# Kernel optimization log

Measured on AMD Instinct MI355X. Metric: run time of the kernel, lower is better.

Reference implementation:

```python
import jax, jax.numpy as jnp
import numpy as np

NB, DM, DIN, DS, DTR, K = 4, 64, 128, 16, 4, 4
C, COUT, H, W, BATCH, NH = 256, 256, 32, 32, 4, 8


def layernorm(x, w, b, eps=1e-5):
    mu = x.mean(-1, keepdims=True)
    var = ((x - mu) ** 2).mean(-1, keepdims=True)
    return (x - mu) * jax.lax.rsqrt(var + eps) * w + b


def ln_hw(x, eps=1e-5):
    # F.layer_norm(x, [H, W]) -> normalize over last two dims, no affine
    mu = x.mean((-2, -1), keepdims=True)
    var = ((x - mu) ** 2).mean((-2, -1), keepdims=True)
    return (x - mu) * jax.lax.rsqrt(var + eps)


def conv1d(x, w, b, groups=1, pad=1):
    # x: (B, Cin, L), w: (Cout, Cin//groups, k)
    y = jax.lax.conv_general_dilated(x, w, (1,), [(pad, pad)],
                                     dimension_numbers=('NCH', 'OIH', 'NCH'),
                                     feature_group_count=groups)
    return y + b[None, :, None]


def selective_scan(u, dt, Bm, Cm, A, Dp):
    # u, dt: (B,L,din); Bm, Cm: (B,L,ds); A: (din,ds); Dp: (din,)
    dA = jnp.exp(dt[..., None] * A)                     # (B,L,din,ds)
    dBu = (dt * u)[..., None] * Bm[:, :, None, :]       # (B,L,din,ds)

    def step(h, inp):
        dA_t, dBu_t, C_t = inp
        h = dA_t * h + dBu_t
        return h, jnp.einsum('bds,bs->bd', h, C_t)

    h0 = jnp.zeros((u.shape[0], DIN, DS), u.dtype)
    _, ys = jax.lax.scan(step, h0, (dA.transpose(1, 0, 2, 3), dBu.transpose(1, 0, 2, 3), Cm.transpose(1, 0, 2)))
    return ys.transpose(1, 0, 2) + u * Dp


def mamba(xs, inw, convw, convb, xpw, dtw, dtb, alog, dp, outw):
    # xs: (B,L,DM) one branch of Mamba(d_model=DM, d_state=DS, d_conv=K, expand=2)
    xz = xs @ inw.T                                     # (B,L,2*DIN)
    u, z = jnp.split(xz, 2, axis=-1)
    # causal depthwise conv1d (torch pads K-1 and truncates to L == left pad K-1)
    uc = jax.lax.conv_general_dilated(u.transpose(0, 2, 1), convw[:, None, :], (1,), [(K - 1, 0)],
                                      dimension_numbers=('NCH', 'OIH', 'NCH'),
                                      feature_group_count=DIN) + convb[None, :, None]
    u = jax.nn.silu(uc.transpose(0, 2, 1))              # (B,L,DIN)
    xdbc = u @ xpw.T                                    # (B,L,DTR+2*DS)
    dt = jax.nn.softplus(xdbc[..., :DTR] @ dtw.T + dtb)
    Bm, Cm = xdbc[..., DTR:DTR + DS], xdbc[..., DTR + DS:]
    y = selective_scan(u, dt, Bm, Cm, -jnp.exp(alog), dp)
    return (y * jax.nn.silu(z)) @ outw.T


mamba_v = jax.vmap(mamba)  # over branch axis 0 of inputs and all params


def mha(x, inw, inb, outw, outb):
    B, N, Cc = x.shape
    hd = Cc // NH
    qkv = x @ inw.T + inb
    q, k, v = jnp.split(qkv, 3, axis=-1)
    q = q.reshape(B, N, NH, hd).transpose(0, 2, 1, 3)
    k = k.reshape(B, N, NH, hd).transpose(0, 2, 1, 3)
    v = v.reshape(B, N, NH, hd).transpose(0, 2, 1, 3)
    att = jax.nn.softmax((q @ k.transpose(0, 1, 3, 2)) * (1.0 / (hd ** 0.5)), axis=-1)
    o = (att @ v).transpose(0, 2, 1, 3).reshape(B, N, Cc)
    return o @ outw.T + outb


def reference(x, norm_w, norm_b, skip_scale, m_inw, m_convw, m_convb, m_xpw, m_dtw, m_dtb, m_alog, m_d, m_outw, qdw_w, qdw_b, qpw_w, qpw_b, rdw_w, rdw_b, rpw_w, rpw_b, fdw_w, fdw_b, fpw_w, fpw_b, lc_w, lc_b, attn_inw, attn_inb, attn_outw, attn_outb, lgn_w, lgn_b, fc_w, fc_b, dwc_w, dwc_b, proj_w, proj_b):
    B, Cc, Hh, Ww = x.shape
    N = Hh * Ww
    xs = x.reshape(B, Cc, N).transpose(0, 2, 1)         # (B,N,C)
    xn = layernorm(xs, norm_w, norm_b)
    # channel-chunk into NB branches: (NB,B,N,DM)
    xc = xn.reshape(B, N, NB, DM).transpose(2, 0, 1, 3)
    xm = mamba_v(xc, m_inw, m_convw, m_convb, m_xpw, m_dtw, m_dtb, m_alog, m_d, m_outw) + skip_scale * xc
    x_concat = xm.transpose(1, 2, 0, 3).reshape(B, N, Cc)
    # branch gating: depthwise grouped conv (C->NB) then pointwise (NB->NB)
    Q = conv1d(conv1d(x_concat.transpose(0, 2, 1), qdw_w, qdw_b, groups=NB, pad=1), qpw_w, qpw_b, groups=1, pad=0)
    g = jax.nn.sigmoid(Q)                               # (B,NB,N)
    xg = (g.transpose(1, 0, 2)[..., None] * xm).transpose(1, 2, 0, 3).reshape(B, N, Cc)
    xgt = xg.transpose(0, 2, 1)                          # (B,C,N)
    R = conv1d(conv1d(xgt, rdw_w, rdw_b, groups=Cc, pad=1), rpw_w, rpw_b, groups=1, pad=0) + xgt
    cat = jnp.concatenate([xs, R.transpose(0, 2, 1)], axis=-1).transpose(0, 2, 1)  # (B,2C,N)
    xm2 = conv1d(conv1d(cat, fdw_w, fdw_b, groups=2 * Cc, pad=1), fpw_w, fpw_b, groups=1, pad=0) + cat[:, :Cc, :]
    xm2 = xm2.transpose(0, 2, 1)                         # (B,N,C)
    # local-global feature mixing
    x_local = conv1d(xm2.transpose(0, 2, 1), lc_w, lc_b, groups=Cc, pad=1).transpose(0, 2, 1)
    x_global = mha(xm2, attn_inw, attn_inb, attn_outw, attn_outb)
    x_out = jnp.concatenate([x_local, x_global], axis=-1) @ fc_w.T + fc_b
    x_out = jax.nn.gelu(layernorm(x_out, lgn_w, lgn_b), approximate=False)
    # DepthwiseConvolution: layer_norm over [H,W] (no affine) then depthwise conv2d
    xi = x_out.transpose(0, 2, 1).reshape(B, Cc, Hh, Ww)
    xi = ln_hw(xi)
    xi = jax.lax.conv_general_dilated(xi, dwc_w, (1, 1), [(1, 1), (1, 1)],
                                      dimension_numbers=('NCHW', 'OIHW', 'NCHW'),
                                      feature_group_count=Cc) + dwc_b[None, :, None, None]
    x_mixed = xi.reshape(B, Cc, N).transpose(0, 2, 1)
    x_mixed = layernorm(x_mixed, norm_w, norm_b)        # self.norm reused
    x_mixed = x_mixed @ proj_w.T + proj_b
    return x_mixed.transpose(0, 2, 1).reshape(B, COUT, Hh, Ww)


def setup_inputs() -> dict:
    key = jax.random.key(0)
    ks = iter(jax.random.split(key, 64))

    def rn(shape, s=0.02):
        return jax.random.normal(next(ks), shape, jnp.float32) * s

    return dict(
        x=jax.random.normal(next(ks), (BATCH, C, H, W), jnp.float32),
        norm_w=jnp.ones((C,), jnp.float32), norm_b=jnp.zeros((C,), jnp.float32),
        skip_scale=jnp.ones((1,), jnp.float32),
        m_inw=rn((NB, 2 * DIN, DM)), m_convw=rn((NB, DIN, K), 0.2), m_convb=jnp.zeros((NB, DIN), jnp.float32),
        m_xpw=rn((NB, DTR + 2 * DS, DIN)), m_dtw=rn((NB, DIN, DTR), 0.2), m_dtb=rn((NB, DIN), 0.5),
        m_alog=jnp.tile(jnp.log(jnp.arange(1, DS + 1, dtype=jnp.float32)), (NB, DIN, 1)),
        m_d=jnp.ones((NB, DIN), jnp.float32), m_outw=rn((NB, DM, DIN)),
        qdw_w=rn((NB, C // NB, 3), 0.1), qdw_b=jnp.zeros((NB,), jnp.float32),
        qpw_w=rn((NB, NB, 1), 0.3), qpw_b=jnp.zeros((NB,), jnp.float32),
        rdw_w=rn((C, 1, 3), 0.2), rdw_b=jnp.zeros((C,), jnp.float32),
        rpw_w=rn((C, C, 1)), rpw_b=jnp.zeros((C,), jnp.float32),
        fdw_w=rn((2 * C, 1, 3), 0.2), fdw_b=jnp.zeros((2 * C,), jnp.float32),
        fpw_w=rn((C, 2 * C, 1)), fpw_b=jnp.zeros((C,), jnp.float32),
        lc_w=rn((C, 1, 3), 0.2), lc_b=jnp.zeros((C,), jnp.float32),
        attn_inw=rn((3 * C, C)), attn_inb=jnp.zeros((3 * C,), jnp.float32),
        attn_outw=rn((C, C)), attn_outb=jnp.zeros((C,), jnp.float32),
        lgn_w=jnp.ones((C,), jnp.float32), lgn_b=jnp.zeros((C,), jnp.float32),
        fc_w=rn((C, 2 * C)), fc_b=jnp.zeros((C,), jnp.float32),
        dwc_w=rn((C, 1, 3, 3), 0.2), dwc_b=jnp.zeros((C,), jnp.float32),
        proj_w=rn((COUT, C)), proj_b=jnp.zeros((COUT,), jnp.float32),
    )
```

## Files before the change

### kernel.cpp

```cpp
#include <hip/hip_runtime.h>
#include <math.h>


namespace {
constexpr int NB_ = 4, DM_ = 64, DIN_ = 128, DS_ = 16, DTR_ = 4;
constexpr int C_ = 256, N_ = 1024, B_ = 4, HD_ = 32;
constexpr int NCH = 16, LCH = 64;
constexpr int NSTATE = 16 * 128 * 16;
}

typedef __attribute__((ext_vector_type(8))) short bf16x8;
typedef __attribute__((ext_vector_type(4))) float f32x4;
typedef __attribute__((ext_vector_type(8))) unsigned short ushort8v;
typedef __attribute__((ext_vector_type(4))) unsigned short ushort4v;

__device__ __forceinline__ unsigned short f2b(float f) {
  unsigned int u = __float_as_uint(f);
  unsigned int r = u + 0x7FFFu + ((u >> 16) & 1u);
  return (unsigned short)(r >> 16);
}

__device__ __forceinline__ float siluf(float x) { return x / (1.f + expf(-x)); }
__device__ __forceinline__ float sigmf(float x) { return 1.f / (1.f + expf(-x)); }
__device__ __forceinline__ float softplusf(float x) {
  return fmaxf(x, 0.f) + log1pf(expf(-fabsf(x)));
}

__global__ __launch_bounds__(256) void k_ln_t2(const float* __restrict__ in,
                                               const float* __restrict__ w,
                                               const float* __restrict__ bias,
                                               float* __restrict__ out_ln,
                                               float* __restrict__ out_copy) {
  __shared__ float tile[256][17];
  __shared__ float redp[16][16][2];
  __shared__ float stats[16][2];
  int bx = blockIdx.x;
  int b = bx >> 6, n0 = (bx & 63) * 16;
  int c = threadIdx.x;
  {
    const float* p = in + ((long)(b * C_ + c)) * N_ + n0;
#pragma unroll
    for (int j = 0; j < 16; ++j) tile[c][j] = p[j];
  }
  __syncthreads();
  {
    int n = c & 15, g = c >> 4;
    float a = 0.f, q = 0.f;
#pragma unroll
    for (int i = 0; i < 16; ++i) {
      float v = tile[g * 16 + i][n];
      a += v; q += v * v;
    }
    redp[g][n][0] = a; redp[g][n][1] = q;
  }
  __syncthreads();
  if (c < 16) {
    float a = 0.f, q = 0.f;
#pragma unroll
    for (int g2 = 0; g2 < 16; ++g2) { a += redp[g2][c][0]; q += redp[g2][c][1]; }
    float mu = a * (1.f / C_);
    float rs = rsqrtf(q * (1.f / C_) - mu * mu + 1e-5f);
    stats[c][0] = mu; stats[c][1] = rs;
  }
  __syncthreads();
  float wv = w[c], bv = bias[c];
#pragma unroll
  for (int j = 0; j < 16; ++j) {
    float v = tile[c][j];
    long o = ((long)(b * N_ + n0 + j)) * C_ + c;
    if (out_copy) out_copy[o] = v;
    out_ln[o] = (v - stats[j][0]) * stats[j][1] * wv + bv;
  }
}

__global__ __launch_bounds__(256) void k_inproj_mfma(const float* __restrict__ xn,
                                                     const float* __restrict__ inw,
                                                     float* __restrict__ UPRE,
                                                     float* __restrict__ Z) {
  __shared__ unsigned short xa[64][72];
  __shared__ unsigned short wb[64][72];
  int r0 = blockIdx.x * 64;
  int nb = blockIdx.y >> 2, c0 = (blockIdx.y & 3) * 64;
  int t = threadIdx.x;
  int wv = t >> 6, lane = t & 63, g = lane >> 4, ql = lane & 15;
  const f32x4 zf = {0.f, 0.f, 0.f, 0.f};
  f32x4 acc[4] = {zf, zf, zf, zf};
  int rr = t >> 2, kq = (t & 3) * 16;
  {
    const float* xsrc = xn + (long)(r0 + rr) * C_ + nb * 64 + kq;
#pragma unroll
    for (int j = 0; j < 4; ++j) {
      float4 v = *(const float4*)(xsrc + 4 * j);
      ushort4v u = {f2b(v.x), f2b(v.y), f2b(v.z), f2b(v.w)};
      *(ushort4v*)&xa[rr][kq + 4 * j] = u;
    }
    const float* wsrc = inw + ((long)nb * 256 + c0 + rr) * 64 + kq;
#pragma unroll
    for (int j = 0; j < 4; ++j) {
      float4 v = *(const float4*)(wsrc + 4 * j);
      ushort4v u = {f2b(v.x), f2b(v.y), f2b(v.z), f2b(v.w)};
      *(ushort4v*)&wb[rr][kq + 4 * j] = u;
    }
// ... 23 lines not shown
__global__ __launch_bounds__(256) void k_causal(const float* __restrict__ Uin,
                                                float* __restrict__ Uout,
                                                const float* __restrict__ cw,
                                                const float* __restrict__ cb) {
  __shared__ float u_s[35][128];
  int bx = blockIdx.x;
  int nbb = bx >> 5, chk = bx & 31;
  int nb = nbb >> 2;
  int n0 = chk * 32;
  const float* ibase = Uin + (long)nbb * N_ * DIN_;
  float* obase = Uout + (long)nbb * N_ * DIN_;
  for (int i = threadIdx.x; i < 35 * 32; i += 256) {
    int row = i >> 5, q = i & 31;
    int n = n0 - 3 + row;
    float4 v = (n >= 0) ? *(const float4*)&ibase[(long)n * DIN_ + q * 4]
                        : make_float4(0.f, 0.f, 0.f, 0.f);
    *(float4*)&u_s[row][q * 4] = v;
  }
  __syncthreads();
  int d = threadIdx.x & 127, half = threadIdx.x >> 7;
  float w0 = cw[(nb * DIN_ + d) * 4 + 0], w1 = cw[(nb * DIN_ + d) * 4 + 1];
  float w2 = cw[(nb * DIN_ + d) * 4 + 2], w3 = cw[(nb * DIN_ + d) * 4 + 3];
  float bv = cb[nb * DIN_ + d];
#pragma unroll
  for (int j = 0; j < 16; ++j) {
    int nn = half * 16 + j;
    float acc = bv + w3 * u_s[nn + 3][d] + w2 * u_s[nn + 2][d] +
                w1 * u_s[nn + 1][d] + w0 * u_s[nn][d];
    obase[(long)(n0 + nn) * DIN_ + d] = siluf(acc);
  }
}

__global__ __launch_bounds__(256) void k_xdbc(const float* __restrict__ U,
                                              const float* __restrict__ xpw,
                                              const float* __restrict__ dtw,
                                              const float* __restrict__ dtb,
                                              float* __restrict__ DT,
                                              float* __restrict__ BMb, float* __restrict__ CMb) {
  __shared__ float wl[36][129];
  __shared__ float u16[16][129];
  __shared__ float xd_s[16][37];
  __shared__ float dtw_s[128][4];
  __shared__ float dtb_s[128];
  int t = threadIdx.x;
  long row0 = (long)blockIdx.x * 16;
  int nb = blockIdx.x >> 8;
  for (int i = t; i < 36 * 128; i += 256) wl[i >> 7][i & 127] = xpw[nb * 36 * 128 + i];
  for (int i = t; i < 16 * 128; i += 256) u16[i >> 7][i & 127] = U[(row0 + (i >> 7)) * DIN_ + (i & 127)];
  for (int i = t; i < 512; i += 256) dtw_s[i >> 2][i & 3] = dtw[nb * 512 + i];
  if (t < 128) dtb_s[t] = dtb[nb * DIN_ + t];
  __syncthreads();
  {
    int r = t >> 4, jl = t & 15;
    float a0 = 0.f, a1 = 0.f, a2 = 0.f;
    for (int k = 0; k < 128; ++k) {
      float uv = u16[r][k];
      a0 += uv * wl[jl][k];
      a1 += uv * wl[jl + 16][k];
      if (jl < 4) a2 += uv * wl[jl + 32][k];
    }
    xd_s[r][jl] = a0;
    xd_s[r][jl + 16] = a1;
    if (jl < 4) xd_s[r][jl + 32] = a2;
  }
  __syncthreads();
  {
    int r = t >> 4, s = t & 15;
    BMb[(row0 + r) * DS_ + s] = xd_s[r][4 + s];
    CMb[(row0 + r) * DS_ + s] = xd_s[r][20 + s];
  }
  {
    int r = t >> 4, dl = t & 15;
    float x0 = xd_s[r][0], x1 = xd_s[r][1], x2 = xd_s[r][2], x3 = xd_s[r][3];
#pragma unroll
    for (int dd = 0; dd < 8; ++dd) {
      int d = dl * 8 + dd;
      float a = dtb_s[d] + x0 * dtw_s[d][0] + x1 * dtw_s[d][1] +
                x2 * dtw_s[d][2] + x3 * dtw_s[d][3];
      DT[(row0 + r) * DIN_ + d] = softplusf(a);
    }
  }
}

__global__ __launch_bounds__(256) void k_scanA(const float* __restrict__ DT,
                                               const float* __restrict__ U,
                                               const float* __restrict__ BMb,
                                               const float* __restrict__ alog,
                                               float* __restrict__ Aprod,
                                               float* __restrict__ Hend) {
  __shared__ float dt_s[64][64];
  __shared__ float u_s[64][64];
  __shared__ float bm_s[64][16];
  int bx = blockIdx.x;
  int chunk = bx >> 5, rem = bx & 31, nbb = rem >> 1, dh = rem & 1;
  int nb = nbb >> 2;
  int t = threadIdx.x;
  int dl = t >> 2, sg = t & 3;
  int d = dh * 64 + dl;
  long base = (long)nbb * N_ + chunk * LCH;
#pragma unroll
  for (int j = 0; j < 4; ++j) {
    int f = t + 256 * j;
    int tt = f >> 4, dq = (f & 15) * 4;
    long src = (base + tt) * DIN_ + dh * 64 + dq;
    *(float4*)&dt_s[tt][dq] = *(const float4*)&DT[src];
    *(float4*)&u_s[tt][dq]  = *(const float4*)&U[src];
  }
  {
    int tt = t >> 2, sq = (t & 3) * 4;
    *(float4*)&bm_s[tt][sq] = *(const float4*)&BMb[(base + tt) * DS_ + sq];
  }
  float A[4];
#pragma unroll
  for (int i = 0; i < 4; ++i)
    A[i] = -expf(alog[(nb * DIN_ + d) * DS_ + sg * 4 + i]);
  __syncthreads();
  float h[4] = {0.f, 0.f, 0.f, 0.f};
  float ap[4] = {1.f, 1.f, 1.f, 1.f};
  for (int tt = 0; tt < LCH; ++tt) {
    float dtv = dt_s[tt][dl];
    float uv  = u_s[tt][dl];
    float cc = dtv * uv;
    float4 bm4 = *(const float4*)&bm_s[tt][sg * 4];
    float bmv[4] = {bm4.x, bm4.y, bm4.z, bm4.w};
#pragma unroll
    for (int i = 0; i < 4; ++i) {
      float dA = __expf(dtv * A[i]);
      h[i] = dA * h[i] + cc * bmv[i];
      ap[i] *= dA;
    }
  }
  long st = (long)chunk * NSTATE + ((nbb << 7) + d) * 16 + sg * 4;
  *(float4*)&Aprod[st] = make_float4(ap[0], ap[1], ap[2], ap[3]);
  *(float4*)&Hend[st]  = make_float4(h[0], h[1], h[2], h[3]);
}

__global__ __launch_bounds__(256) void k_scanB(float* __restrict__ Aprod,
                                               const float* __restrict__ Hend) {
  int state = blockIdx.x * 256 + threadIdx.x;
  float H = 0.f;
#pragma unroll
  for (int c = 0; c < NCH; ++c) {
    long idx = (long)c * NSTATE + state;
    float a = Aprod[idx];
    float e = Hend[idx];
    Aprod[idx] = H;
    H = e + a * H;
  }
}

__global__ __launch_bounds__(256) void k_scanC(float* __restrict__ DT,
                                               const float* __restrict__ U,
                                               const float* __restrict__ BMb,
                                               const float* __restrict__ CMb,
                                               const float* __restrict__ alog,
                                               const float* __restrict__ Dp,
                                               const float* __restrict__ Hin) {
  __shared__ float dt_s[64][64];
  __shared__ float u_s[64][64];
  __shared__ float bm_s[64][16];
  __shared__ float cm_s[64][16];
  int bx = blockIdx.x;
  int chunk = bx >> 5, rem = bx & 31, nbb = rem >> 1, dh = rem & 1;
  int nb = nbb >> 2;
  int t = threadIdx.x;
  int dl = t >> 2, sg = t & 3;
  int d = dh * 64 + dl;
  long base = (long)nbb * N_ + chunk * LCH;
#pragma unroll
  for (int j = 0; j < 4; ++j) {
    int f = t + 256 * j;
    int tt = f >> 4, dq = (f & 15) * 4;
    long src = (base + tt) * DIN_ + dh * 64 + dq;
    *(float4*)&dt_s[tt][dq] = *(const float4*)&DT[src];
    *(float4*)&u_s[tt][dq]  = *(const float4*)&U[src];
  }
  {
    int tt = t >> 2, sq = (t & 3) * 4;
    *(float4*)&bm_s[tt][sq] = *(const float4*)&BMb[(base + tt) * DS_ + sq];
    *(float4*)&cm_s[tt][sq] = *(const float4*)&CMb[(base + tt) * DS_ + sq];
  }
  float A[4];
#pragma unroll
  for (int i = 0; i < 4; ++i)
    A[i] = -expf(alog[(nb * DIN_ + d) * DS_ + sg * 4 + i]);
  float Dv = Dp[nb * DIN_ + d];
  float h[4];
  {
    long st = (long)chunk * NSTATE + ((nbb << 7) + d) * 16 + sg * 4;
    float4 h4 = *(const float4*)&Hin[st];
    h[0] = h4.x; h[1] = h4.y; h[2] = h4.z; h[3] = h4.w;
  }
  __syncthreads();
  for (int tt = 0; tt < LCH; ++tt) {
    float dtv = dt_s[tt][dl];
    float uv  = u_s[tt][dl];
    float cc = dtv * uv;
    float4 bm4 = *(const float4*)&bm_s[tt][sg * 4];
    float4 cm4 = *(const float4*)&cm_s[tt][sg * 4];
    float bmv[4] = {bm4.x, bm4.y, bm4.z, bm4.w};
    float cmv[4] = {cm4.x, cm4.y, cm4.z, cm4.w};
    float p = 0.f;
#pragma unroll
    for (int i = 0; i < 4; ++i) {
      float dA = __expf(dtv * A[i]);
      h[i] = dA * h[i] + cc * bmv[i];
      p += h[i] * cmv[i];
    }
    p += __shfl_xor(p, 1, 64);
    p += __shfl_xor(p, 2, 64);
    if (sg == 0) DT[(base + tt) * DIN_ + d] = p + Dv * uv;
  }
}

__global__ __launch_bounds__(256) void k_outproj_mfma(const float* __restrict__ Y,
                                                      const float* __restrict__ Zb,
                                                      const float* __restrict__ outw,
                                                      const float* __restrict__ xn,
                                                      const float* __restrict__ skip,
                                                      float* __restrict__ XMC) {
  __shared__ unsigned short xa[64][72];
  __shared__ unsigned short wb[64][72];
  int r0 = blockIdx.x * 64;
  int nb = blockIdx.y;
  int t = threadIdx.x;
  int wv = t >> 6, lane = t & 63, g = lane >> 4, ql = lane & 15;
  const f32x4 zf = {0.f, 0.f, 0.f, 0.f};
  f32x4 acc[4] = {zf, zf, zf, zf};
  int rr = t >> 2, kq = (t & 3) * 16;
  for (int k0 = 0; k0 < 128; k0 += 64) {
    __syncthreads();
    long row = (long)nb * 4096 + r0 + rr;
    const float* ysrc = Y + row * DIN_ + k0 + kq;
    const float* zsrc = Zb + row * DIN_ + k0 + kq;
#pragma unroll
    for (int j = 0; j < 4; ++j) {
      float4 yv = *(const float4*)(ysrc + 4 * j);
      float4 zv = *(const float4*)(zsrc + 4 * j);
      ushort4v u = {f2b(yv.x * siluf(zv.x)), f2b(yv.y * siluf(zv.y)),
                    f2b(yv.z * siluf(zv.z)), f2b(yv.w * siluf(zv.w))};
      *(ushort4v*)&xa[rr][kq + 4 * j] = u;
    }
    const float* wsrc = outw + ((long)nb * 64 + rr) * 128 + k0 + kq;
#pragma unroll
    for (int j = 0; j < 4; ++j) {
      float4 v = *(const float4*)(wsrc + 4 * j);
      ushort4v u = {f2b(v.x), f2b(v.y), f2b(v.z), f2b(v.w)};
      *(ushort4v*)&wb[rr][kq + 4 * j] = u;
    }
    __syncthreads();
#pragma unroll
    for (int ks = 0; ks < 2; ++ks) {
      bf16x8 a = *(const bf16x8*)&xa[wv * 16 + ql][ks * 32 + g * 8];
#pragma unroll
      for (int ct = 0; ct < 4; ++ct) {
        bf16x8 b = *(const bf16x8*)&wb[ct * 16 + ql][ks * 32 + g * 8];
        acc[ct] = __builtin_amdgcn_mfma_f32_16x16x32_bf16(a, b, acc[ct], 0, 0, 0);
      }
    }
  }
  float sk = skip[0];
#pragma unroll
  for (int ct = 0; ct < 4; ++ct) {
    int col = ct * 16 + ql;
#pragma unroll
    for (int reg = 0; reg < 4; ++reg) {
      int bn = r0 + wv * 16 + g * 4 + reg;
      long oc = (long)bn * C_ + nb * 64 + col;
      XMC[oc] = acc[ct][reg] + sk * xn[oc];
    }
  }
}

__global__ __launch_bounds__(256) void k_gate(const float* __restrict__ XMC,
                                              const float* __restrict__ qdw_w,
                                              const float* __restrict__ qdw_b,
                                              const float* __restrict__ qpw_w,
                                              const float* __restrict__ qpw_b,
                                              float* __restrict__ G) {
  int t = threadIdx.x;
  int gid = (blockIdx.x * 256 + t) >> 4;
  int cq = t & 3, p = (t >> 2) & 3;
  int b = gid >> 10, n = gid & 1023;
  float a = 0.f;
#pragma unroll
  for (int k = 0; k < 3; ++k) {
    int nn = n + k - 1;
    if (nn < 0 || nn >= N_) continue;
    const float* xr = XMC + ((long)b * N_ + nn) * C_ + p * 64 + cq * 16;
    const float* wr = qdw_w + (p * 64 + cq * 16) * 3 + k;
#pragma unroll
    for (int i = 0; i < 16; ++i) a += xr[i] * wr[i * 3];
  }
  a += __shfl_xor(a, 1, 64);
// ... 118 lines not shown
  }
}

template <int KD, bool TOUT>
__global__ __launch_bounds__(256) void k_gemm_rm(const float* __restrict__ inA,
                                                 const float* __restrict__ inB,
                                                 const float* __restrict__ w,
                                                 const float* __restrict__ bias,
                                                 float* __restrict__ out,
                                                 int Cout, int lda) {
  __shared__ unsigned short xa[64][72];
  __shared__ unsigned short wb[64][72];
  __shared__ float tt[TOUT ? 64 : 1][TOUT ? 68 : 1];
  int r0 = blockIdx.x * 64;
  int c0 = blockIdx.y * 64;
  int t = threadIdx.x;
  int wv = t >> 6, lane = t & 63, g = lane >> 4, ql = lane & 15;
  const f32x4 zf = {0.f, 0.f, 0.f, 0.f};
  f32x4 acc[4] = {zf, zf, zf, zf};
  int rr = t >> 2, kq = (t & 3) * 16;
  for (int k0 = 0; k0 < KD; k0 += 64) {
    __syncthreads();
    int kk = k0 + kq;
    const float* xsrc = (inB != nullptr && kk >= KD / 2)
                            ? inB + (long)(r0 + rr) * lda + (kk - KD / 2)
                            : inA + (long)(r0 + rr) * lda + kk;
#pragma unroll
    for (int j = 0; j < 4; ++j) {
      float4 v = *(const float4*)(xsrc + 4 * j);
      ushort4v u = {f2b(v.x), f2b(v.y), f2b(v.z), f2b(v.w)};
      *(ushort4v*)&xa[rr][kq + 4 * j] = u;
    }
    const float* wsrc = w + (long)(c0 + rr) * KD + kk;
#pragma unroll
    for (int j = 0; j < 4; ++j) {
      float4 v = *(const float4*)(wsrc + 4 * j);
      ushort4v u = {f2b(v.x), f2b(v.y), f2b(v.z), f2b(v.w)};
      *(ushort4v*)&wb[rr][kq + 4 * j] = u;
    }
    __syncthreads();
#pragma unroll
    for (int ks = 0; ks < 2; ++ks) {
      bf16x8 a = *(const bf16x8*)&xa[wv * 16 + ql][ks * 32 + g * 8];
#pragma unroll
      for (int ct = 0; ct < 4; ++ct) {
        bf16x8 b = *(const bf16x8*)&wb[ct * 16 + ql][ks * 32 + g * 8];
        acc[ct] = __builtin_amdgcn_mfma_f32_16x16x32_bf16(a, b, acc[ct], 0, 0, 0);
      }
    }
  }
  if constexpr (!TOUT) {
#pragma unroll
    for (int ct = 0; ct < 4; ++ct) {
      int col = c0 + ct * 16 + ql;
      float bv = bias[col];
#pragma unroll
      for (int reg = 0; reg < 4; ++reg) {
        long row = r0 + wv * 16 + g * 4 + reg;
        out[row * Cout + col] = acc[ct][reg] + bv;
      }
    }
  } else {
#pragma unroll
    for (int ct = 0; ct < 4; ++ct) {
      int col = ct * 16 + ql;
      float bv = bias[c0 + col];
#pragma unroll
      for (int reg = 0; reg < 4; ++reg)
        tt[col][wv * 16 + g * 4 + reg] = acc[ct][reg] + bv;
    }
    __syncthreads();
    int b = r0 >> 10, n0 = r0 & 1023;
    int col = t >> 2, nq = (t & 3) * 16;
    float* op = out + ((long)(b * 256 + c0 + col)) * 1024 + n0 + nq;
#pragma unroll
    for (int j = 0; j < 4; ++j) {
      float4 v = make_float4(tt[col][nq + 4 * j], tt[col][nq + 4 * j + 1],
                             tt[col][nq + 4 * j + 2], tt[col][nq + 4 * j + 3]);
      *(float4*)(op + 4 * j) = v;
    }
  }
}

__global__ __launch_bounds__(256) void k_gemm_fc(const float* __restrict__ XM2,
                                                 const float* __restrict__ XGL,
                                                 const float* __restrict__ lcw,
                                                 const float* __restrict__ lcb,
                                                 const float* __restrict__ w,
                                                 const float* __restrict__ bias,
                                                 float* __restrict__ out) {
  __shared__ unsigned short xa[64][72];
  __shared__ unsigned short wb[64][72];
  int r0 = blockIdx.x * 64;
  int c0 = blockIdx.y * 64;
  int t = threadIdx.x;
  int wv = t >> 6, lane = t & 63, g = lane >> 4, ql = lane & 15;
  const f32x4 zf = {0.f, 0.f, 0.f, 0.f};
  f32x4 acc[4] = {zf, zf, zf, zf};
  int rr = t >> 2, kq = (t & 3) * 16;
  for (int k0 = 0; k0 < 512; k0 += 64) {
    __syncthreads();
    int kk = k0 + kq;
    long row = r0 + rr;
    if (kk < 256) {
      int n = (int)(row & 1023);
      const float* pc = XM2 + row * 256 + kk;
      bool hm = n > 0, hp = n < 1023;
#pragma unroll
      for (int j = 0; j < 4; ++j) {
        float4 v = *(const float4*)(pc + 4 * j);
        float4 vm = hm ? *(const float4*)(pc - 256 + 4 * j) : make_float4(0.f, 0.f, 0.f, 0.f);
        float4 vp = hp ? *(const float4*)(pc + 256 + 4 * j) : make_float4(0.f, 0.f, 0.f, 0.f);
        int c = kk + 4 * j;
        xa[rr][kq + 4 * j + 0] = f2b(lcb[c + 0] + lcw[(c + 0) * 3] * vm.x + lcw[(c + 0) * 3 + 1] * v.x + lcw[(c + 0) * 3 + 2] * vp.x);
        xa[rr][kq + 4 * j + 1] = f2b(lcb[c + 1] + lcw[(c + 1) * 3] * vm.y + lcw[(c + 1) * 3 + 1] * v.y + lcw[(c + 1) * 3 + 2] * vp.y);
        xa[rr][kq + 4 * j + 2] = f2b(lcb[c + 2] + lcw[(c + 2) * 3] * vm.z + lcw[(c + 2) * 3 + 1] * v.z + lcw[(c + 2) * 3 + 2] * vp.z);
        xa[rr][kq + 4 * j + 3] = f2b(lcb[c + 3] + lcw[(c + 3) * 3] * vm.w + lcw[(c + 3) * 3 + 1] * v.w + lcw[(c + 3) * 3 + 2] * vp.w);
      }
    } else {
      const float* xsrc = XGL + row * 256 + (kk - 256);
#pragma unroll
      for (int j = 0; j < 4; ++j) {
        float4 v = *(const float4*)(xsrc + 4 * j);
        ushort4v u = {f2b(v.x), f2b(v.y), f2b(v.z), f2b(v.w)};
        *(ushort4v*)&xa[rr][kq + 4 * j] = u;
      }
    }
    const float* wsrc = w + (long)(c0 + rr) * 512 + kk;
#pragma unroll
    for (int j = 0; j < 4; ++j) {
      float4 v = *(const float4*)(wsrc + 4 * j);
      ushort4v u = {f2b(v.x), f2b(v.y), f2b(v.z), f2b(v.w)};
      *(ushort4v*)&wb[rr][kq + 4 * j] = u;
    }
    __syncthreads();
#pragma unroll
    for (int ks = 0; ks < 2; ++ks) {
      bf16x8 a = *(const bf16x8*)&xa[wv * 16 + ql][ks * 32 + g * 8];
#pragma unroll
      for (int ct = 0; ct < 4; ++ct) {
        bf16x8 b = *(const bf16x8*)&wb[ct * 16 + ql][ks * 32 + g * 8];
        acc[ct] = __builtin_amdgcn_mfma_f32_16x16x32_bf16(a, b, acc[ct], 0, 0, 0);
      }
    }
  }
#pragma unroll
  for (int ct = 0; ct < 4; ++ct) {
    int col = c0 + ct * 16 + ql;
    float bv = bias[col];
#pragma unroll
    for (int reg = 0; reg < 4; ++reg) {
      long row = r0 + wv * 16 + g * 4 + reg;
      out[row * 256 + col] = acc[ct][reg] + bv;
    }
  }
}

__global__ __launch_bounds__(256) void k_attn_mfma(const float* __restrict__ qkv,
                                                   float* __restrict__ O) {
  __shared__ unsigned short K_lds[64 * 40];
  __shared__ unsigned short Vt_lds[32 * 72];
  __shared__ unsigned short P_lds[4][16 * 72];
  int bx = blockIdx.x;
  int bh = bx >> 4, qt = bx & 15;
  int b = bh >> 3, h = bh & 7;
  int t = threadIdx.x;
  int w = t >> 6, lane = t & 63;
  int g = lane >> 4, ql = lane & 15;
  const float qscale = 0.17677669529663687f * 1.44269504088896341f;

  bf16x8 q_frag;
  {
    const float* qp = qkv + ((long)(b * N_ + qt * 64 + w * 16 + ql)) * 768 + h * HD_ + g * 8;
#pragma unroll
    for (int i = 0; i < 8; ++i) q_frag[i] = (short)f2b(qp[i] * qscale);
  }
  float m = -1e30f, l = 0.f;
  f32x4 o_acc[2];
  const f32x4 zf = {0.f, 0.f, 0.f, 0.f};
  o_acc[0] = zf; o_acc[1] = zf;

  for (int kt = 0; kt < 16; ++kt) {
    __syncthreads();
    {
      int kr = t >> 2, d0 = (t & 3) * 8;
      const float* gp = qkv + ((long)(b * N_ + kt * 64 + kr)) * 768 + 256 + h * HD_ + d0;
      ushort8v kv;
#pragma unroll
      for (int i = 0; i < 8; ++i) kv[i] = f2b(gp[i]);
      *(ushort8v*)&K_lds[kr * 40 + d0] = kv;
      const float* vp = gp + 256;
#pragma unroll
      for (int i = 0; i < 8; ++i) Vt_lds[(d0 + i) * 72 + kr] = f2b(vp[i]);
    }
    __syncthreads();
    f32x4 s_frag[4];
#pragma unroll
    for (int s = 0; s < 4; ++s) {
      bf16x8 k_frag = *(const bf16x8*)&K_lds[(s * 16 + ql) * 40 + g * 8];
      s_frag[s] = __builtin_amdgcn_mfma_f32_16x16x32_bf16(k_frag, q_frag, zf, 0, 0, 0);
    }
    float sv[16];
#pragma unroll
    for (int s = 0; s < 4; ++s)
#pragma unroll
      for (int r = 0; r < 4; ++r) sv[s * 4 + r] = s_frag[s][r];
    float tmax = sv[0];
#pragma unroll
    for (int i = 1; i < 16; ++i) tmax = fmaxf(tmax, sv[i]);
    tmax = fmaxf(tmax, __shfl_xor(tmax, 16));
    tmax = fmaxf(tmax, __shfl_xor(tmax, 32));
    float mn = fmaxf(m, tmax);
    float corr = exp2f(m - mn);
    float psum = 0.f;
    unsigned short pb[16];
#pragma unroll
    for (int i = 0; i < 16; ++i) {
      float p = exp2f(sv[i] - mn);
      psum += p;
      pb[i] = f2b(p);
    }
    psum += __shfl_xor(psum, 16);
    psum += __shfl_xor(psum, 32);
    l = l * corr + psum;
    m = mn;
#pragma unroll
    for (int mt = 0; mt < 2; ++mt)
#pragma unroll
      for (int r = 0; r < 4; ++r) o_acc[mt][r] *= corr;
#pragma unroll
    for (int s = 0; s < 4; ++s) {
      ushort4v p4 = {pb[s * 4], pb[s * 4 + 1], pb[s * 4 + 2], pb[s * 4 + 3]};
      *(ushort4v*)&P_lds[w][ql * 72 + s * 16 + g * 4] = p4;
    }
#pragma unroll
    for (int c = 0; c < 2; ++c) {
      bf16x8 p_frag = *(const bf16x8*)&P_lds[w][ql * 72 + c * 32 + g * 8];
#pragma unroll
      for (int mt = 0; mt < 2; ++mt) {
        bf16x8 v_frag = *(const bf16x8*)&Vt_lds[(mt * 16 + ql) * 72 + c * 32 + g * 8];
        o_acc[mt] = __builtin_amdgcn_mfma_f32_16x16x32_bf16(v_frag, p_frag, o_acc[mt], 0, 0, 0);
      }
    }
  }
  float inv = 1.f / l;
  float* op = O + ((long)(b * N_ + qt * 64 + w * 16 + ql)) * C_ + h * HD_;
#pragma unroll
  for (int mt = 0; mt < 2; ++mt) {
    float4 o4 = make_float4(o_acc[mt][0] * inv, o_acc[mt][1] * inv,
                            o_acc[mt][2] * inv, o_acc[mt][3] * inv);
    *(float4*)(op + mt * 16 + g * 4) = o4;
  }
}

__global__ __launch_bounds__(256) void k_lngelu(const float* __restrict__ XO,
                                                const float* __restrict__ lw,
                                                const float* __restrict__ lb,
                                                float* __restrict__ XI) {
  __shared__ float tile[256][17];
  __shared__ float redp[16][16][2];
  __shared__ float stats[16][2];
  int bx = blockIdx.x;
  int b = bx >> 6, n0 = (bx & 63) * 16;
  int c = threadIdx.x;
#pragma unroll
  for (int j = 0; j < 16; ++j)
    tile[c][j] = XO[((long)(b * N_ + n0 + j)) * C_ + c];
  __syncthreads();
  {
    int n = c & 15, g = c >> 4;
    float a = 0.f, q = 0.f;
#pragma unroll
    for (int i = 0; i < 16; ++i) {
      float v = tile[g * 16 + i][n];
      a += v; q += v * v;
    }
    redp[g][n][0] = a; redp[g][n][1] = q;
  }
  __syncthreads();
  if (c < 16) {
    float a = 0.f, q = 0.f;
#pragma unroll
    for (int g2 = 0; g2 < 16; ++g2) { a += redp[g2][c][0]; q += redp[g2][c][1]; }
    float mu = a * (1.f / C_);
    float rs = rsqrtf(q * (1.f / C_) - mu * mu + 1e-5f);
    stats[c][0] = mu; stats[c][1] = rs;
  }
  __syncthreads();
  float wv = lw[c], bv = lb[c];
  float o[16];
#pragma unroll
  for (int j = 0; j < 16; ++j) {
    float x = (tile[c][j] - stats[j][0]) * stats[j][1] * wv + bv;
    o[j] = 0.5f * x * (1.f + erff(x * 0.70710678118654752f));
  }
  float* dst = &XI[((long)(b * C_ + c)) * N_ + n0];
#pragma unroll
  for (int j4 = 0; j4 < 4; ++j4)
    *(float4*)(dst + j4 * 4) = make_float4(o[4 * j4], o[4 * j4 + 1], o[4 * j4 + 2], o[4 * j4 + 3]);
}

__global__ __launch_bounds__(256) void k_lnhw(float* __restrict__ XI) {
  __shared__ float red[8];
  long base = (long)blockIdx.x * N_;
  float a = 0.f, b2 = 0.f;
  for (int i = threadIdx.x; i < N_; i += 256) {
    float v = XI[base + i];
    a += v; b2 += v * v;
  }
#pragma unroll
  for (int m = 1; m < 64; m <<= 1) {
    a += __shfl_xor(a, m, 64);
    b2 += __shfl_xor(b2, m, 64);
  }
  int w = threadIdx.x >> 6;
  if ((threadIdx.x & 63) == 0) { red[2 * w] = a; red[2 * w + 1] = b2; }
  __syncthreads();
  float sa = red[0] + red[2] + red[4] + red[6];
  float sq = red[1] + red[3] + red[5] + red[7];
  float mu = sa * (1.f / N_);
  float rs = rsqrtf(sq * (1.f / N_) - mu * mu + 1e-5f);
  for (int i = threadIdx.x; i < N_; i += 256) XI[base + i] = (XI[base + i] - mu) * rs;
}

__global__ __launch_bounds__(256) void k_dwc(const float* __restrict__ XI,
                                             const float* __restrict__ w,
                                             const float* __restrict__ bias,
                                             float* __restrict__ XD) {
  long i = (long)blockIdx.x * 256 + threadIdx.x;
  int hw = i & 1023;
  int wq = hw & 31, hq = hw >> 5;
  int c = (int)((i >> 10) & 255);
  const float* p = XI + (i - hw);
  const float* wk = w + c * 9;
  float a = bias[c];
#pragma unroll
  for (int kh = 0; kh < 3; ++kh) {
    int h2 = hq + kh - 1;
    if (h2 < 0 || h2 >= 32) continue;
#pragma unroll
    for (int kw = 0; kw < 3; ++kw) {
      int w2 = wq + kw - 1;
      if (w2 < 0 || w2 >= 32) continue;
      a += wk[kh * 3 + kw] * p[h2 * 32 + w2];
    }
  }
  XD[i] = a;
}

extern "C" void kernel_launch(void* const* d_in, const int* in_sizes, int n_in,
                              void* d_out, int out_size, void* d_ws, size_t ws_size,
                              hipStream_t stream) {
  const float* x        = (const float*)d_in[0];
  const float* norm_w   = (const float*)d_in[1];
  const float* norm_b   = (const float*)d_in[2];
  const float* skip     = (const float*)d_in[3];
  const float* m_inw    = (const float*)d_in[4];
  const float* m_convw  = (const float*)d_in[5];
  const float* m_convb  = (const float*)d_in[6];
  const float* m_xpw    = (const float*)d_in[7];
  const float* m_dtw    = (const float*)d_in[8];
  const float* m_dtb    = (const float*)d_in[9];
  const float* m_alog   = (const float*)d_in[10];
  const float* m_d      = (const float*)d_in[11];
  const float* m_outw   = (const float*)d_in[12];
  const float* qdw_w    = (const float*)d_in[13];
  const float* qdw_b    = (const float*)d_in[14];
  const float* qpw_w    = (const float*)d_in[15];
  const float* qpw_b    = (const float*)d_in[16];
  const float* rdw_w    = (const float*)d_in[17];
  const float* rdw_b    = (const float*)d_in[18];
  const float* rpw_w    = (const float*)d_in[19];
  const float* rpw_b    = (const float*)d_in[20];
  const float* fdw_w    = (const float*)d_in[21];
  const float* fdw_b    = (const float*)d_in[22];
  const float* fpw_w    = (const float*)d_in[23];
  const float* fpw_b    = (const float*)d_in[24];
  const float* lc_w     = (const float*)d_in[25];
  const float* lc_b     = (const float*)d_in[26];
  const float* attn_inw = (const float*)d_in[27];
  const float* attn_inb = (const float*)d_in[28];
  const float* attn_outw= (const float*)d_in[29];
  const float* attn_outb= (const float*)d_in[30];
  const float* lgn_w    = (const float*)d_in[31];
  const float* lgn_b    = (const float*)d_in[32];
  const float* fc_w     = (const float*)d_in[33];
  const float* fc_b     = (const float*)d_in[34];
  const float* dwc_w    = (const float*)d_in[35];
  const float* dwc_b    = (const float*)d_in[36];
  const float* proj_w   = (const float*)d_in[37];
  const float* proj_b   = (const float*)d_in[38];
  float* out = (float*)d_out;

  float* ws = (float*)d_ws;
  const size_t F = 1048576;
  float* XS  = ws + 0 * F;
  float* XN  = ws + 1 * F;
  float* U   = ws + 2 * F;
  float* Z   = ws + 4 * F;
  float* UPRE= ws + 6 * F;
  float* DT  = ws + 6 * F;
  float* BM  = ws + 8 * F;
  float* CM  = ws + 8 * F + F / 4;
  float* XMC = ws + 8 * F + F / 2;
  float* SC_APROD = ws + 8 * F + F / 2;
  float* SC_HEND  = ws + 9 * F;
  float* G   = ws + 1 * F;
  float* XG  = ws + 2 * F;
  float* RB  = ws + 4 * F;
  float* XM2 = ws + 5 * F;
  float* QKV = ws + 1 * F;
  float* O   = ws + 4 * F;
  float* XGL = ws + 6 * F;
  float* XO  = ws + 7 * F;
  float* XI  = ws + 8 * F;
  float* XD  = ws + 5 * F;
  float* LNF = ws + 0 * F;
  (void)ws_size; (void)in_sizes; (void)n_in; (void)out_size;

  k_ln_t2<<<256, 256, 0, stream>>>(x, norm_w, norm_b, XN, XS);
  k_inproj_mfma<<<dim3(64, 16), 256, 0, stream>>>(XN, m_inw, UPRE, Z);
  k_causal<<<512, 256, 0, stream>>>(UPRE, U, m_convw, m_convb);
  k_xdbc<<<1024, 256, 0, stream>>>(U, m_xpw, m_dtw, m_dtb, DT, BM, CM);
  k_scanA<<<512, 256, 0, stream>>>(DT, U, BM, m_alog, SC_APROD, SC_HEND);
  k_scanB<<<128, 256, 0, stream>>>(SC_APROD, SC_HEND);
  k_scanC<<<512, 256, 0, stream>>>(DT, U, BM, CM, m_alog, m_d, SC_APROD);
  k_outproj_mfma<<<dim3(64, 4), 256, 0, stream>>>(DT, Z, m_outw, XN, skip, XMC);
  k_gate<<<256, 256, 0, stream>>>(XMC, qdw_w, qdw_b, qpw_w, qpw_b, G);
  k_xg<<<256, 256, 0, stream>>>(XMC, G, XG);
  k_gemm_cm_dw<256><<<dim3(64, 4), 256, 0, stream>>>(XG, nullptr, rdw_w, rdw_b,
                                                     rpw_w, rpw_b, XG, nullptr, RB, nullptr);
  k_gemm_cm_dw<512><<<dim3(64, 4), 256, 0, stream>>>(x, RB, fdw_w, fdw_b,
                                                     fpw_w, fpw_b, nullptr, XS, nullptr, XM2);
  k_gemm_rm<256, false><<<dim3(64, 12), 256, 0, stream>>>(XM2, nullptr, attn_inw, attn_inb, QKV, 768, 256);
  k_attn_mfma<<<512, 256, 0, stream>>>(QKV, O);
  k_gemm_rm<256, false><<<dim3(64, 4), 256, 0, stream>>>(O, nullptr, attn_outw, attn_outb, XGL, 256, 256);
  k_gemm_fc<<<dim3(64, 4), 256, 0, stream>>>(XM2, XGL, lc_w, lc_b, fc_w, fc_b, XO);
  k_lngelu<<<256, 256, 0, stream>>>(XO, lgn_w, lgn_b, XI);
  k_lnhw<<<1024, 256, 0, stream>>>(XI);
  k_dwc<<<4096, 256, 0, stream>>>(XI, dwc_w, dwc_b, XD);
  k_ln_t2<<<256, 256, 0, stream>>>(XD, norm_w, norm_b, LNF, nullptr);
  k_gemm_rm<256, true><<<dim3(64, 4), 256, 0, stream>>>(LNF, nullptr, proj_w, proj_b, out, 256, 256);
}
```

Measured before the change: 224.8 us.

## Fuse scan into cooperative kernel, emit bf16 QKV, fuse spatial LN with depthwise conv

Merges the three chunked selective-scan kernels into one cooperative launch that uses grid-wide syncs between the local scan, the cross-chunk carry pass and the output pass, so the chunk data stays in LDS instead of being reloaded. Adds a dedicated QKV GEMM that writes bf16 directly, which lets attention load vectors without converting; the softmax scale moves from Q to the scores. The spatial layernorm is fused with the 3x3 depthwise conv through a shared-memory plane, which removes one pass over that tensor and one launch. The cooperative launch needs all 512 blocks resident at once, and grid syncs carry their own overhead.

```diff
diff --git a/kernel.cpp b/kernel.cpp
--- a/kernel.cpp
+++ b/kernel.cpp
@@ -1,6 +1,9 @@
 #include <hip/hip_runtime.h>
+#include <hip/hip_cooperative_groups.h>
 #include <math.h>
 
+
+namespace cg = cooperative_groups;
 
 namespace {
 constexpr int NB_ = 4, DM_ = 64, DIN_ = 128, DS_ = 16, DTR_ = 4;
@@ -18,6 +21,20 @@
   unsigned int u = __float_as_uint(f);
   unsigned int r = u + 0x7FFFu + ((u >> 16) & 1u);
   return (unsigned short)(r >> 16);
+}
+
+__device__ __forceinline__ float2 blockReduce2(float a, float b, float* red) {
+#pragma unroll
+  for (int m = 1; m < 64; m <<= 1) {
+    a += __shfl_xor(a, m, 64);
+    b += __shfl_xor(b, m, 64);
+  }
+  int w = threadIdx.x >> 6;
+  if ((threadIdx.x & 63) == 0) { red[2 * w] = a; red[2 * w + 1] = b; }
+  __syncthreads();
+  float ra = red[0] + red[2] + red[4] + red[6];
+  float rb = red[1] + red[3] + red[5] + red[7];
+  return make_float2(ra, rb);
 }
 
 __device__ __forceinline__ float siluf(float x) { return x / (1.f + expf(-x)); }
@@ -207,15 +224,19 @@
   }
 }
 
-__global__ __launch_bounds__(256) void k_scanA(const float* __restrict__ DT,
-                                               const float* __restrict__ U,
-                                               const float* __restrict__ BMb,
-                                               const float* __restrict__ alog,
-                                               float* __restrict__ Aprod,
-                                               float* __restrict__ Hend) {
+__global__ __launch_bounds__(256) void k_scan_coop(float* __restrict__ DT,
+                                                   const float* __restrict__ U,
+                                                   const float* __restrict__ BMb,
+                                                   const float* __restrict__ CMb,
+                                                   const float* __restrict__ alog,
+                                                   const float* __restrict__ Dp,
+                                                   float* __restrict__ Aprod,
+                                                   float* __restrict__ Hend) {
   __shared__ float dt_s[64][64];
   __shared__ float u_s[64][64];
   __shared__ float bm_s[64][16];
+  __shared__ float cm_s[64][16];
+  cg::grid_group grid = cg::this_grid();
   int bx = blockIdx.x;
   int chunk = bx >> 5, rem = bx & 31, nbb = rem >> 1, dh = rem & 1;
   int nb = nbb >> 2;
@@ -234,75 +255,6 @@
   {
     int tt = t >> 2, sq = (t & 3) * 4;
     *(float4*)&bm_s[tt][sq] = *(const float4*)&BMb[(base + tt) * DS_ + sq];
-  }
-  float A[4];
-#pragma unroll
-  for (int i = 0; i < 4; ++i)
-    A[i] = -expf(alog[(nb * DIN_ + d) * DS_ + sg * 4 + i]);
-  __syncthreads();
-  float h[4] = {0.f, 0.f, 0.f, 0.f};
-  float ap[4] = {1.f, 1.f, 1.f, 1.f};
-  for (int tt = 0; tt < LCH; ++tt) {
-    float dtv = dt_s[tt][dl];
-    float uv  = u_s[tt][dl];
-    float cc = dtv * uv;
-    float4 bm4 = *(const float4*)&bm_s[tt][sg * 4];
-    float bmv[4] = {bm4.x, bm4.y, bm4.z, bm4.w};
-#pragma unroll
-    for (int i = 0; i < 4; ++i) {
-      float dA = __expf(dtv * A[i]);
-      h[i] = dA * h[i] + cc * bmv[i];
-      ap[i] *= dA;
-    }
-  }
-  long st = (long)chunk * NSTATE + ((nbb << 7) + d) * 16 + sg * 4;
-  *(float4*)&Aprod[st] = make_float4(ap[0], ap[1], ap[2], ap[3]);
-  *(float4*)&Hend[st]  = make_float4(h[0], h[1], h[2], h[3]);
-}
-
-__global__ __launch_bounds__(256) void k_scanB(float* __restrict__ Aprod,
-                                               const float* __restrict__ Hend) {
-  int state = blockIdx.x * 256 + threadIdx.x;
-  float H = 0.f;
-#pragma unroll
-  for (int c = 0; c < NCH; ++c) {
-    long idx = (long)c * NSTATE + state;
-    float a = Aprod[idx];
-    float e = Hend[idx];
-    Aprod[idx] = H;
-    H = e + a * H;
-  }
-}
-
-__global__ __launch_bounds__(256) void k_scanC(float* __restrict__ DT,
-                                               const float* __restrict__ U,
-                                               const float* __restrict__ BMb,
-                                               const float* __restrict__ CMb,
-                                               const float* __restrict__ alog,
-                                               const float* __restrict__ Dp,
-                                               const float* __restrict__ Hin) {
-  __shared__ float dt_s[64][64];
-  __shared__ float u_s[64][64];
-  __shared__ float bm_s[64][16];
-  __shared__ float cm_s[64][16];
-  int bx = blockIdx.x;
-  int chunk = bx >> 5, rem = bx & 31, nbb = rem >> 1, dh = rem & 1;
-  int nb = nbb >> 2;
-  int t = threadIdx.x;
-  int dl = t >> 2, sg = t & 3;
-  int d = dh * 64 + dl;
-  long base = (long)nbb * N_ + chunk * LCH;
-#pragma unroll
-  for (int j = 0; j < 4; ++j) {
-    int f = t + 256 * j;
-    int tt = f >> 4, dq = (f & 15) * 4;
-    long src = (base + tt) * DIN_ + dh * 64 + dq;
-    *(float4*)&dt_s[tt][dq] = *(const float4*)&DT[src];
-    *(float4*)&u_s[tt][dq]  = *(const float4*)&U[src];
-  }
-  {
-    int tt = t >> 2, sq = (t & 3) * 4;
-    *(float4*)&bm_s[tt][sq] = *(const float4*)&BMb[(base + tt) * DS_ + sq];
     *(float4*)&cm_s[tt][sq] = *(const float4*)&CMb[(base + tt) * DS_ + sq];
   }
   float A[4];
@@ -310,31 +262,68 @@
   for (int i = 0; i < 4; ++i)
     A[i] = -expf(alog[(nb * DIN_ + d) * DS_ + sg * 4 + i]);
   float Dv = Dp[nb * DIN_ + d];
-  float h[4];
-  {
-    long st = (long)chunk * NSTATE + ((nbb << 7) + d) * 16 + sg * 4;
-    float4 h4 = *(const float4*)&Hin[st];
+  long st = (long)chunk * NSTATE + ((nbb << 7) + d) * 16 + sg * 4;
+  __syncthreads();
+  {
+    float h[4] = {0.f, 0.f, 0.f, 0.f};
+    float ap[4] = {1.f, 1.f, 1.f, 1.f};
+    for (int tt = 0; tt < LCH; ++tt) {
+      float dtv = dt_s[tt][dl];
+      float uv  = u_s[tt][dl];
+      float cc = dtv * uv;
+      float4 bm4 = *(const float4*)&bm_s[tt][sg * 4];
+      float bmv[4] = {bm4.x, bm4.y, bm4.z, bm4.w};
+#pragma unroll
+      for (int i = 0; i < 4; ++i) {
+        float dA = __expf(dtv * A[i]);
+        h[i] = dA * h[i] + cc * bmv[i];
+        ap[i] *= dA;
+      }
+    }
+    *(float4*)&Aprod[st] = make_float4(ap[0], ap[1], ap[2], ap[3]);
+    *(float4*)&Hend[st]  = make_float4(h[0], h[1], h[2], h[3]);
+  }
+  __threadfence();
+  grid.sync();
+  {
+    int gid = bx * 256 + t;
+    if (gid < NSTATE) {
+      float H = 0.f;
+#pragma unroll
+      for (int c = 0; c < NCH; ++c) {
+        long idx = (long)c * NSTATE + gid;
+        float a = Aprod[idx];
+        float e = Hend[idx];
+        Aprod[idx] = H;
+        H = e + a * H;
+      }
+    }
+  }
+  __threadfence();
+  grid.sync();
+  {
+    float h[4];
+    float4 h4 = *(const float4*)&Aprod[st];
     h[0] = h4.x; h[1] = h4.y; h[2] = h4.z; h[3] = h4.w;
-  }
-  __syncthreads();
-  for (int tt = 0; tt < LCH; ++tt) {
-    float dtv = dt_s[tt][dl];
-    float uv  = u_s[tt][dl];
-    float cc = dtv * uv;
-    float4 bm4 = *(const float4*)&bm_s[tt][sg * 4];
-    float4 cm4 = *(const float4*)&cm_s[tt][sg * 4];
-    float bmv[4] = {bm4.x, bm4.y, bm4.z, bm4.w};
-    float cmv[4] = {cm4.x, cm4.y, cm4.z, cm4.w};
-    float p = 0.f;
-#pragma unroll
-    for (int i = 0; i < 4; ++i) {
-      float dA = __expf(dtv * A[i]);
-      h[i] = dA * h[i] + cc * bmv[i];
-      p += h[i] * cmv[i];
-    }
-    p += __shfl_xor(p, 1, 64);
-    p += __shfl_xor(p, 2, 64);
-    if (sg == 0) DT[(base + tt) * DIN_ + d] = p + Dv * uv;
+    for (int tt = 0; tt < LCH; ++tt) {
+      float dtv = dt_s[tt][dl];
+      float uv  = u_s[tt][dl];
+      float cc = dtv * uv;
+      float4 bm4 = *(const float4*)&bm_s[tt][sg * 4];
+      float4 cm4 = *(const float4*)&cm_s[tt][sg * 4];
+      float bmv[4] = {bm4.x, bm4.y, bm4.z, bm4.w};
+      float cmv[4] = {cm4.x, cm4.y, cm4.z, cm4.w};
+      float p = 0.f;
+#pragma unroll
+      for (int i = 0; i < 4; ++i) {
+        float dA = __expf(dtv * A[i]);
+        h[i] = dA * h[i] + cc * bmv[i];
+        p += h[i] * cmv[i];
+      }
+      p += __shfl_xor(p, 1, 64);
+      p += __shfl_xor(p, 2, 64);
+      if (sg == 0) DT[(base + tt) * DIN_ + d] = p + Dv * uv;
+    }
   }
 }
 
@@ -619,6 +608,58 @@
   }
 }
 
+__global__ __launch_bounds__(256) void k_gemm_qkv(const float* __restrict__ in,
+                                                  const float* __restrict__ w,
+                                                  const float* __restrict__ bias,
+                                                  unsigned short* __restrict__ out) {
+  __shared__ unsigned short xa[64][72];
+  __shared__ unsigned short wb[64][72];
+  int r0 = blockIdx.x * 64;
+  int c0 = blockIdx.y * 64;
+  int t = threadIdx.x;
+  int wv = t >> 6, lane = t & 63, g = lane >> 4, ql = lane & 15;
+  const f32x4 zf = {0.f, 0.f, 0.f, 0.f};
+  f32x4 acc[4] = {zf, zf, zf, zf};
+  int rr = t >> 2, kq = (t & 3) * 16;
+  for (int k0 = 0; k0 < 256; k0 += 64) {
+    __syncthreads();
+    const float* xsrc = in + (long)(r0 + rr) * 256 + k0 + kq;
+#pragma unroll
+    for (int j = 0; j < 4; ++j) {
+      float4 v = *(const float4*)(xsrc + 4 * j);
+      ushort4v u = {f2b(v.x), f2b(v.y), f2b(v.z), f2b(v.w)};
+      *(ushort4v*)&xa[rr][kq + 4 * j] = u;
+    }
+    const float* wsrc = w + (long)(c0 + rr) * 256 + k0 + kq;
+#pragma unroll
+    for (int j = 0; j < 4; ++j) {
+      float4 v = *(const float4*)(wsrc + 4 * j);
+      ushort4v u = {f2b(v.x), f2b(v.y), f2b(v.z), f2b(v.w)};
+      *(ushort4v*)&wb[rr][kq + 4 * j] = u;
+    }
+    __syncthreads();
+#pragma unroll
+    for (int ks = 0; ks < 2; ++ks) {
+      bf16x8 a = *(const bf16x8*)&xa[wv * 16 + ql][ks * 32 + g * 8];
+#pragma unroll
+      for (int ct = 0; ct < 4; ++ct) {
+        bf16x8 b = *(const bf16x8*)&wb[ct * 16 + ql][ks * 32 + g * 8];
+        acc[ct] = __builtin_amdgcn_mfma_f32_16x16x32_bf16(a, b, acc[ct], 0, 0, 0);
+      }
+    }
+  }
+#pragma unroll
+  for (int ct = 0; ct < 4; ++ct) {
+    int col = c0 + ct * 16 + ql;
+    float bv = bias[col];
+#pragma unroll
+    for (int reg = 0; reg < 4; ++reg) {
+      long row = r0 + wv * 16 + g * 4 + reg;
+      out[row * 768 + col] = f2b(acc[ct][reg] + bv);
+    }
+  }
+}
+
 __global__ __launch_bounds__(256) void k_gemm_fc(const float* __restrict__ XM2,
                                                  const float* __restrict__ XGL,
                                                  const float* __restrict__ lcw,
@@ -693,7 +734,7 @@
   }
 }
 
-__global__ __launch_bounds__(256) void k_attn_mfma(const float* __restrict__ qkv,
+__global__ __launch_bounds__(256) void k_attn_mfma(const unsigned short* __restrict__ qkvb,
                                                    float* __restrict__ O) {
   __shared__ unsigned short K_lds[64 * 40];
   __shared__ unsigned short Vt_lds[32 * 72];
@@ -706,12 +747,7 @@
   int g = lane >> 4, ql = lane & 15;
   const float qscale = 0.17677669529663687f * 1.44269504088896341f;
 
-  bf16x8 q_frag;
-  {
-    const float* qp = qkv + ((long)(b * N_ + qt * 64 + w * 16 + ql)) * 768 + h * HD_ + g * 8;
-#pragma unroll
-    for (int i = 0; i < 8; ++i) q_frag[i] = (short)f2b(qp[i] * qscale);
-  }
+  bf16x8 q_frag = *(const bf16x8*)(qkvb + ((long)(b * N_ + qt * 64 + w * 16 + ql)) * 768 + h * HD_ + g * 8);
   float m = -1e30f, l = 0.f;
   f32x4 o_acc[2];
   const f32x4 zf = {0.f, 0.f, 0.f, 0.f};
@@ -721,14 +757,12 @@
     __syncthreads();
     {
       int kr = t >> 2, d0 = (t & 3) * 8;
-      const float* gp = qkv + ((long)(b * N_ + kt * 64 + kr)) * 768 + 256 + h * HD_ + d0;
-      ushort8v kv;
-#pragma unroll
-      for (int i = 0; i < 8; ++i) kv[i] = f2b(gp[i]);
+      const unsigned short* gp = qkvb + ((long)(b * N_ + kt * 64 + kr)) * 768 + 256 + h * HD_ + d0;
+      ushort8v kv = *(const ushort8v*)gp;
       *(ushort8v*)&K_lds[kr * 40 + d0] = kv;
-      const float* vp = gp + 256;
-#pragma unroll
-      for (int i = 0; i < 8; ++i) Vt_lds[(d0 + i) * 72 + kr] = f2b(vp[i]);
+      ushort8v vv = *(const ushort8v*)(gp + 256);
+#pragma unroll
+      for (int i = 0; i < 8; ++i) Vt_lds[(d0 + i) * 72 + kr] = vv[i];
     }
     __syncthreads();
     f32x4 s_frag[4];
@@ -741,7 +775,7 @@
 #pragma unroll
     for (int s = 0; s < 4; ++s)
 #pragma unroll
-      for (int r = 0; r < 4; ++r) sv[s * 4 + r] = s_frag[s][r];
+      for (int r = 0; r < 4; ++r) sv[s * 4 + r] = s_frag[s][r] * qscale;
     float tmax = sv[0];
 #pragma unroll
     for (int i = 1; i < 16; ++i) tmax = fmaxf(tmax, sv[i]);
@@ -837,52 +871,50 @@
     *(float4*)(dst + j4 * 4) = make_float4(o[4 * j4], o[4 * j4 + 1], o[4 * j4 + 2], o[4 * j4 + 3]);
 }
 
-__global__ __launch_bounds__(256) void k_lnhw(float* __restrict__ XI) {
+__global__ __launch_bounds__(256) void k_lnhw_dwc(const float* __restrict__ XIin,
+                                                  const float* __restrict__ w,
+                                                  const float* __restrict__ bias,
+                                                  float* __restrict__ XD) {
+  __shared__ float pl[32][33];
   __shared__ float red[8];
-  long base = (long)blockIdx.x * N_;
-  float a = 0.f, b2 = 0.f;
-  for (int i = threadIdx.x; i < N_; i += 256) {
-    float v = XI[base + i];
-    a += v; b2 += v * v;
-  }
-#pragma unroll
-  for (int m = 1; m < 64; m <<= 1) {
-    a += __shfl_xor(a, m, 64);
-    b2 += __shfl_xor(b2, m, 64);
-  }
-  int w = threadIdx.x >> 6;
-  if ((threadIdx.x & 63) == 0) { red[2 * w] = a; red[2 * w + 1] = b2; }
-  __syncthreads();
-  float sa = red[0] + red[2] + red[4] + red[6];
-  float sq = red[1] + red[3] + red[5] + red[7];
-  float mu = sa * (1.f / N_);
-  float rs = rsqrtf(sq * (1.f / N_) - mu * mu + 1e-5f);
-  for (int i = threadIdx.x; i < N_; i += 256) XI[base + i] = (XI[base + i] - mu) * rs;
-}
-
-__global__ __launch_bounds__(256) void k_dwc(const float* __restrict__ XI,
-                                             const float* __restrict__ w,
-                                             const float* __restrict__ bias,
-                                             float* __restrict__ XD) {
-  long i = (long)blockIdx.x * 256 + threadIdx.x;
-  int hw = i & 1023;
-  int wq = hw & 31, hq = hw >> 5;
-  int c = (int)((i >> 10) & 255);
-  const float* p = XI + (i - hw);
-  const float* wk = w + c * 9;
-  float a = bias[c];
-#pragma unroll
-  for (int kh = 0; kh < 3; ++kh) {
-    int h2 = hq + kh - 1;
-    if (h2 < 0 || h2 >= 32) continue;
-#pragma unroll
-    for (int kw = 0; kw < 3; ++kw) {
-      int w2 = wq + kw - 1;
-      if (w2 < 0 || w2 >= 32) continue;
-      a += wk[kh * 3 + kw] * p[h2 * 32 + w2];
-    }
-  }
-  XD[i] = a;
+  long base = (long)blockIdx.x * 1024;
+  int c = blockIdx.x & 255;
+  int t = threadIdx.x;
+  float4 v = *(const float4*)&XIin[base + t * 4];
+  float a = v.x + v.y + v.z + v.w;
+  float q = v.x * v.x + v.y * v.y + v.z * v.z + v.w * v.w;
+  float2 s = blockReduce2(a, q, red);
+  float mu = s.x * (1.f / 1024.f);
+  float rs = rsqrtf(s.y * (1.f / 1024.f) - mu * mu + 1e-5f);
+  int hh = t >> 3, w0 = (t & 7) * 4;
+  pl[hh][w0 + 0] = (v.x - mu) * rs;
+  pl[hh][w0 + 1] = (v.y - mu) * rs;
+  pl[hh][w0 + 2] = (v.z - mu) * rs;
+  pl[hh][w0 + 3] = (v.w - mu) * rs;
+  __syncthreads();
+  float wk[9];
+#pragma unroll
+  for (int i = 0; i < 9; ++i) wk[i] = w[c * 9 + i];
+  float bv = bias[c];
+  float o[4];
+#pragma unroll
+  for (int j = 0; j < 4; ++j) {
+    int ww = w0 + j;
+    float acc = bv;
+#pragma unroll
+    for (int kh = 0; kh < 3; ++kh) {
+      int h2 = hh + kh - 1;
+      if (h2 < 0 || h2 >= 32) continue;
+#pragma unroll
+      for (int kw = 0; kw < 3; ++kw) {
+        int w2 = ww + kw - 1;
+        if (w2 < 0 || w2 >= 32) continue;
+        acc += wk[kh * 3 + kw] * pl[h2][w2];
+      }
+    }
+    o[j] = acc;
+  }
+  *(float4*)&XD[base + t * 4] = make_float4(o[0], o[1], o[2], o[3]);
 }
 
 extern "C" void kernel_launch(void* const* d_in, const int* in_sizes, int n_in,
@@ -946,7 +978,7 @@
   float* XG  = ws + 2 * F;
   float* RB  = ws + 4 * F;
   float* XM2 = ws + 5 * F;
-  float* QKV = ws + 1 * F;
+  unsigned short* QKVB = (unsigned short*)(ws + 1 * F);
   float* O   = ws + 4 * F;
   float* XGL = ws + 6 * F;
   float* XO  = ws + 7 * F;
@@ -959,9 +991,11 @@
   k_inproj_mfma<<<dim3(64, 16), 256, 0, stream>>>(XN, m_inw, UPRE, Z);
   k_causal<<<512, 256, 0, stream>>>(UPRE, U, m_convw, m_convb);
   k_xdbc<<<1024, 256, 0, stream>>>(U, m_xpw, m_dtw, m_dtb, DT, BM, CM);
-  k_scanA<<<512, 256, 0, stream>>>(DT, U, BM, m_alog, SC_APROD, SC_HEND);
-  k_scanB<<<128, 256, 0, stream>>>(SC_APROD, SC_HEND);
-  k_scanC<<<512, 256, 0, stream>>>(DT, U, BM, CM, m_alog, m_d, SC_APROD);
+  {
+    void* cargs[] = {&DT, (void*)&U, (void*)&BM, (void*)&CM,
+                     (void*)&m_alog, (void*)&m_d, &SC_APROD, &SC_HEND};
+    hipLaunchCooperativeKernel((void*)k_scan_coop, dim3(512), dim3(256), cargs, 0, stream);
+  }
   k_outproj_mfma<<<dim3(64, 4), 256, 0, stream>>>(DT, Z, m_outw, XN, skip, XMC);
   k_gate<<<256, 256, 0, stream>>>(XMC, qdw_w, qdw_b, qpw_w, qpw_b, G);
   k_xg<<<256, 256, 0, stream>>>(XMC, G, XG);
@@ -969,13 +1003,12 @@
                                                      rpw_w, rpw_b, XG, nullptr, RB, nullptr);
   k_gemm_cm_dw<512><<<dim3(64, 4), 256, 0, stream>>>(x, RB, fdw_w, fdw_b,
                                                      fpw_w, fpw_b, nullptr, XS, nullptr, XM2);
-  k_gemm_rm<256, false><<<dim3(64, 12), 256, 0, stream>>>(XM2, nullptr, attn_inw, attn_inb, QKV, 768, 256);
-  k_attn_mfma<<<512, 256, 0, stream>>>(QKV, O);
+  k_gemm_qkv<<<dim3(64, 12), 256, 0, stream>>>(XM2, attn_inw, attn_inb, QKVB);
+  k_attn_mfma<<<512, 256, 0, stream>>>(QKVB, O);
   k_gemm_rm<256, false><<<dim3(64, 4), 256, 0, stream>>>(O, nullptr, attn_outw, attn_outb, XGL, 256, 256);
   k_gemm_fc<<<dim3(64, 4), 256, 0, stream>>>(XM2, XGL, lc_w, lc_b, fc_w, fc_b, XO);
   k_lngelu<<<256, 256, 0, stream>>>(XO, lgn_w, lgn_b, XI);
-  k_lnhw<<<1024, 256, 0, stream>>>(XI);
-  k_dwc<<<4096, 256, 0, stream>>>(XI, dwc_w, dwc_b, XD);
+  k_lnhw_dwc<<<1024, 256, 0, stream>>>(XI, dwc_w, dwc_b, XD);
   k_ln_t2<<<256, 256, 0, stream>>>(XD, norm_w, norm_b, LNF, nullptr);
   k_gemm_rm<256, true><<<dim3(64, 4), 256, 0, stream>>>(LNF, nullptr, proj_w, proj_b, out, 256, 256);
 }
```

After: 407.2 us. 81.1% more time.
